# Kernel tuning notes

Measured on AMD Instinct MI355X. Metric: run time of the kernel, lower is better.

The kernel has to match this reference:

```python
import jax, jax.numpy as jnp
import numpy as np

B, N, DIM, PDIM, K = 2, 4096, 512, 64, 16
ALPHA, SIGMA = 0.1, 1.0


def setup_inputs() -> dict:
    key = jax.random.key(0)
    ks = jax.random.split(key, 6)
    sf = 1.0 / np.sqrt(DIM)
    return {
        "states": jax.random.normal(ks[0], (B, N, DIM), jnp.float32),
        "positions": jax.random.normal(ks[1], (B, N, PDIM), jnp.float32),
        "W_flow": jax.random.uniform(ks[2], (PDIM, DIM), jnp.float32, -sf, sf),
        "b_flow": jax.random.uniform(ks[3], (PDIM,), jnp.float32, -sf, sf),
        "W_val": jax.random.uniform(ks[4], (DIM, DIM), jnp.float32, -sf, sf),
        "b_val": jax.random.uniform(ks[5], (DIM,), jnp.float32, -sf, sf),
    }


def _pairwise_dist(p):
    sq = jnp.sum(p * p, axis=-1)  # [B,N]
    d2 = sq[:, :, None] + sq[:, None, :] - 2.0 * jnp.einsum('bnp,bmp->bnm', p, p)
    return jnp.sqrt(jnp.maximum(d2, 1e-12))


def reference(states, positions, W_flow, b_flow, W_val, b_val):
    # flow projection + position update
    flow = jnp.einsum('bnd,pd->bnp', states, W_flow) + b_flow  # [B,N,PDIM]
    new_pos = positions + ALPHA * flow

    # kNN search (exclude self via large diagonal)
    d = _pairwise_dist(new_pos)  # [B,N,N]
    d_knn = d + jnp.eye(N, dtype=d.dtype) * 1e6
    _, nbrs = jax.lax.top_k(-d_knn, K)  # [B,N,K] smallest distances

    # scatter neighbor mask [B,N,N] (no [B,N,K,N] one-hot materialization)
    bidx = jnp.arange(B)[:, None, None]
    ridx = jnp.arange(N)[None, :, None]
    mask = jnp.zeros((B, N, N), d.dtype).at[bidx, ridx, nbrs].set(1.0)

    # gaussian affinities; exp(-d*mask)*mask == exp(-d)*mask on the support
    aff = jnp.exp(-d / (2.0 * SIGMA ** 2)) * mask
    aff = aff / (jnp.sum(aff, axis=-1, keepdims=True) + 1e-8)

    # value projection + weighted aggregation
    values = jnp.einsum('bnd,ed->bne', states, W_val) + b_val  # [B,N,DIM]
    context = jnp.einsum('bnm,bmd->bnd', aff, values)
    return context, new_pos, flow
```

## Files before the change

### kernel.cpp

```cpp
#include <hip/hip_runtime.h>

#define NB 2
#define NN 4096
#define DIMD 512
#define PD 64
#define KNN 16
#define QB 8
#define CAP 192
#define CTRIG 52
#define RCAP 48
#define MROWS (NB*NN)
#define FLOW_BLOCKS (MROWS/4)

typedef unsigned short ushort_t;

__global__ __launch_bounds__(256)
void prep_kernel(const float* __restrict__ states, const float* __restrict__ positions,
                 const float* __restrict__ W_flow, const float* __restrict__ b_flow,
                 const float* __restrict__ W_val, const float* __restrict__ b_val,
                 float* __restrict__ out_np, float* __restrict__ out_fl,
                 float* __restrict__ npos_lo, float* __restrict__ p4t,
                 double* __restrict__ sq64, float* __restrict__ sqf,
                 float* __restrict__ values_ws)
{
    __shared__ __align__(16) unsigned char POOL[24832];
    const int t = threadIdx.x;

    if (blockIdx.x < FLOW_BLOCKS) {
        float (*s_lds)[DIMD] = (float(*)[DIMD])POOL;
        float (*wlds)[65]    = (float(*)[65])(POOL + 8192);
        const int row0 = blockIdx.x * 4;
        const float4* src = (const float4*)(states + (size_t)row0 * DIMD);
        float4* dst = (float4*)&s_lds[0][0];
        dst[t] = src[t];
        dst[t + 256] = src[t + 256];
        const int lr = t >> 6;
        const int p  = t & 63;
        const int row = row0 + lr;
        double a0 = 0.0, a1 = 0.0, a2 = 0.0, a3 = 0.0;
        for (int ph = 0; ph < 8; ++ph) {
            const int d0 = ph << 6;
            __syncthreads();
            #pragma unroll
            for (int i = 0; i < 4; ++i) {
                int slot = t + (i << 8);
                int r = slot >> 4, c = slot & 15;
                float4 wv = *(const float4*)(W_flow + (size_t)r * DIMD + d0 + (c << 2));
                wlds[(c<<2)+0][r] = wv.x;
                wlds[(c<<2)+1][r] = wv.y;
                wlds[(c<<2)+2][r] = wv.z;
                wlds[(c<<2)+3][r] = wv.w;
            }
            __syncthreads();
            #pragma unroll
            for (int sc = 0; sc < 4; ++sc) {
                const int dl = sc << 4;
                float4 s0 = *(const float4*)&s_lds[lr][d0 + dl + 0];
                float4 s1 = *(const float4*)&s_lds[lr][d0 + dl + 4];
                float4 s2 = *(const float4*)&s_lds[lr][d0 + dl + 8];
                float4 s3 = *(const float4*)&s_lds[lr][d0 + dl + 12];
                a0 += (double)s0.x * (double)wlds[dl+ 0][p];
                a1 += (double)s0.y * (double)wlds[dl+ 1][p];
                a2 += (double)s0.z * (double)wlds[dl+ 2][p];
                a3 += (double)s0.w * (double)wlds[dl+ 3][p];
                a0 += (double)s1.x * (double)wlds[dl+ 4][p];
                a1 += (double)s1.y * (double)wlds[dl+ 5][p];
                a2 += (double)s1.z * (double)wlds[dl+ 6][p];
                a3 += (double)s1.w * (double)wlds[dl+ 7][p];
                a0 += (double)s2.x * (double)wlds[dl+ 8][p];
                a1 += (double)s2.y * (double)wlds[dl+ 9][p];
                a2 += (double)s2.z * (double)wlds[dl+10][p];
                a3 += (double)s2.w * (double)wlds[dl+11][p];
                a0 += (double)s3.x * (double)wlds[dl+12][p];
                a1 += (double)s3.y * (double)wlds[dl+13][p];
                a2 += (double)s3.z * (double)wlds[dl+14][p];
                a3 += (double)s3.w * (double)wlds[dl+15][p];
            }
        }
        double acc = ((a0 + a1) + (a2 + a3)) + (double)b_flow[p];
        const size_t g = (size_t)row * PD + p;
        double np_ = (double)positions[g] + 0.1 * acc;
        float hi = (float)np_;
        float lo = (float)(np_ - (double)hi);
        out_fl[g]   = (float)acc;
        out_np[g]   = hi;
        npos_lo[g]  = lo;
        const int bb = row >> 12, n = row & (NN - 1);
        p4t[(((size_t)bb*16 + (p >> 2))*NN + n)*4 + (p & 3)] = hi;
        double s2 = np_ * np_;
        #pragma unroll
        for (int off = 32; off >= 1; off >>= 1) s2 += __shfl_xor(s2, off);
        if (p == 0) { sq64[row] = s2; sqf[row] = (float)s2; }
    } else {
        float (*As)[68] = (float(*)[68])POOL;
        float (*Bs)[68] = (float(*)[68])(POOL + 4352);
        const int idx = blockIdx.x - FLOW_BLOCKS;
        const int bn = idx & 7, bm = idx >> 3;
        const int lr  = t >> 2;
        const int lc4 = (t & 3) << 2;
        const int cr = (t >> 4) << 2;
        const int cc = (t & 15) << 2;
        float acc[4][4] = {};
        for (int k0 = 0; k0 < DIMD; k0 += 16) {
            float4 av = *(const float4*)(states + (size_t)(bm*64 + lr)*DIMD + k0 + lc4);
            float4 wv = *(const float4*)(W_val  + (size_t)(bn*64 + lr)*DIMD + k0 + lc4);
            __syncthreads();
            As[lc4+0][lr] = av.x; As[lc4+1][lr] = av.y; As[lc4+2][lr] = av.z; As[lc4+3][lr] = av.w;
            Bs[lc4+0][lr] = wv.x; Bs[lc4+1][lr] = wv.y; Bs[lc4+2][lr] = wv.z; Bs[lc4+3][lr] = wv.w;
            __syncthreads();
            #pragma unroll
            for (int kk = 0; kk < 16; ++kk) {
                float4 a  = *(const float4*)&As[kk][cr];
                float4 b4 = *(const float4*)&Bs[kk][cc];
                acc[0][0] += a.x*b4.x; acc[0][1] += a.x*b4.y; acc[0][2] += a.x*b4.z; acc[0][3] += a.x*b4.w;
                acc[1][0] += a.y*b4.x; acc[1][1] += a.y*b4.y; acc[1][2] += a.y*b4.z; acc[1][3] += a.y*b4.w;
                acc[2][0] += a.z*b4.x; acc[2][1] += a.z*b4.y; acc[2][2] += a.z*b4.z; acc[2][3] += a.z*b4.w;
                acc[3][0] += a.w*b4.x; acc[3][1] += a.w*b4.y; acc[3][2] += a.w*b4.z; acc[3][3] += a.w*b4.w;
            }
        }
        const int colb = bn*64 + cc;
        float4 bb = *(const float4*)(b_val + colb);
        #pragma unroll
        for (int i = 0; i < 4; ++i) {
            float4 o;
            o.x = acc[i][0] + bb.x;
            o.y = acc[i][1] + bb.y;
            o.z = acc[i][2] + bb.z;
            o.w = acc[i][3] + bb.w;
            *(float4*)(values_ws + (size_t)(bm*64 + cr + i)*DIMD + colb) = o;
        }
    }
}

__global__ __launch_bounds__(256, 4)
void dist_kernel(const float* __restrict__ nph, const float* __restrict__ npl,
                 const float4* __restrict__ p4t, const float* __restrict__ sqf,
                 const double* __restrict__ sq64, const float* __restrict__ values,
                 float* __restrict__ ctx)
{
    __shared__ __align__(16) unsigned char POOL[24576];
    __shared__ float    qstage[QB][68];
    __shared__ ushort_t rlist[QB][4][RCAP];
    __shared__ int      ccnt[QB][4];
    __shared__ int      rcnt[QB][4];

    ushort_t (*sd16)[4][CAP]  = (ushort_t(*)[4][CAP])POOL;
    ushort_t (*six16)[4][CAP] = (ushort_t(*)[4][CAP])(POOL + 12288);
    double (*umbd)[192] = (double(*)[192])POOL;
    int*    umbi        = (int*)(POOL + 12288);
    double (*qd64)[66]  = (double(*)[66])(POOL + 18432);
    int*    fin_ix      = (int*)(POOL + 22656);
    float*  fin_w       = (float*)(POOL + 23168);

    const int tid  = threadIdx.x;
    const int w    = tid >> 6;
    const int lane = tid & 63;
    const int b    = blockIdx.x >> 9;
    const int n0   = (blockIdx.x & 511) << 3;
    const int base = b * NN;

    if (tid < 32) ccnt[tid >> 2][tid & 3] = 0;
    if (tid < 128) {
        int row = tid >> 4, c4 = (tid & 15) << 2;
        *(float4*)&qstage[row][c4] = *(const float4*)(nph + (size_t)(base + n0 + row)*PD + c4);
    }
    __syncthreads();

    float sqq[QB], tv[QB];
    #pragma unroll
    for (int j = 0; j < QB; ++j) { sqq[j] = sqf[base + n0 + j]; tv[j] = 1e30f; }

    const float4* P4 = p4t + (size_t)b * 16 * NN;
    const int qbase = w << 10;

    #define APPEND1(J, DV, CI)                                                  \
        if ((DV) < tv[J]) {                                                     \
            int s_ = atomicAdd(&ccnt[J][w], 1);                                 \
            if (s_ < CAP) {                                                     \
                sd16[J][w][s_]  = (ushort_t)(__float_as_uint(DV) >> 16);        \
                six16[J][w][s_] = (ushort_t)(CI);                               \
            }                                                                   \
        }

    #define COMPACT1(J)                                                         \
        {                                                                       \
            int cnt0 = ccnt[J][w];                                              \
            if (cnt0 > CTRIG) {                                                 \
                if (cnt0 > CAP) cnt0 = CAP;                                     \
                ushort_t v0 = (lane       < cnt0) ? sd16[J][w][lane]       : (ushort_t)0xFFFF; \
                ushort_t v1 = (64 + lane  < cnt0) ? sd16[J][w][64 + lane]  : (ushort_t)0xFFFF; \
                ushort_t v2 = (128 + lane < cnt0) ? sd16[J][w][128 + lane] : (ushort_t)0xFFFF; \
                ushort_t i0 = (lane       < cnt0) ? six16[J][w][lane]       : (ushort_t)0; \
                ushort_t i1 = (64 + lane  < cnt0) ? six16[J][w][64 + lane]  : (ushort_t)0; \
                ushort_t i2 = (128 + lane < cnt0) ? six16[J][w][128 + lane] : (ushort_t)0; \
                unsigned lo_ = 0u, hi_ = 0x7F80u;                               \
                _Pragma("unroll 1")                                             \
                for (int it = 0; it < 16; ++it) {                               \
                    unsigned mid = (lo_ + hi_) >> 1;                            \
                    int cnt = __popcll(__ballot((unsigned)v0 < mid))            \
                            + __popcll(__ballot((unsigned)v1 < mid))            \
                            + __popcll(__ballot((unsigned)v2 < mid));           \
                    if (cnt >= 19) hi_ = mid; else lo_ = mid;                   \
                }                                                               \
                tv[J] = __uint_as_float(hi_ << 16);                             \
                if (lane == 0) ccnt[J][w] = 0;                                  \
                if ((unsigned)v0 < hi_) { int s_ = atomicAdd(&ccnt[J][w], 1); sd16[J][w][s_] = v0; six16[J][w][s_] = i0; } \
                if ((unsigned)v1 < hi_) { int s_ = atomicAdd(&ccnt[J][w], 1); sd16[J][w][s_] = v1; six16[J][w][s_] = i1; } \
                if ((unsigned)v2 < hi_) { int s_ = atomicAdd(&ccnt[J][w], 1); sd16[J][w][s_] = v2; six16[J][w][s_] = i2; } \
            }                                                                   \
        }

    for (int ch = 0; ch < 4; ++ch) {
        const int cbase = qbase + (ch << 8);
        const int c0 = cbase + lane, c1 = c0 + 64, c2 = c0 + 128, c3 = c0 + 192;
        float a[QB][4];
        #pragma unroll
        for (int j = 0; j < QB; ++j) { a[j][0]=0.f; a[j][1]=0.f; a[j][2]=0.f; a[j][3]=0.f; }
        #pragma unroll
        for (int k4 = 0; k4 < 16; ++k4) {
            float4 p0 = P4[(size_t)k4*NN + c0];
            float4 p1 = P4[(size_t)k4*NN + c1];
            float4 p2 = P4[(size_t)k4*NN + c2];
            float4 p3 = P4[(size_t)k4*NN + c3];
            #pragma unroll
            for (int j = 0; j < QB; ++j) {
                float4 qv = *(const float4*)&qstage[j][k4 << 2];
                a[j][0] += qv.x*p0.x + qv.y*p0.y + qv.z*p0.z + qv.w*p0.w;
                a[j][1] += qv.x*p1.x + qv.y*p1.y + qv.z*p1.z + qv.w*p1.w;
                a[j][2] += qv.x*p2.x + qv.y*p2.y + qv.z*p2.z + qv.w*p2.w;
                a[j][3] += qv.x*p3.x + qv.y*p3.y + qv.z*p3.z + qv.w*p3.w;
            }
        }
        const float sc0 = sqf[base + c0], sc1 = sqf[base + c1];
        const float sc2 = sqf[base + c2], sc3 = sqf[base + c3];
        #pragma unroll
        for (int j = 0; j < QB; ++j) {
            float d0 = fmaxf(sqq[j] + sc0 - 2.f*a[j][0], 0.f);
            float d1 = fmaxf(sqq[j] + sc1 - 2.f*a[j][1], 0.f);
            float d2 = fmaxf(sqq[j] + sc2 - 2.f*a[j][2], 0.f);
            float d3 = fmaxf(sqq[j] + sc3 - 2.f*a[j][3], 0.f);
            if (c0 == n0 + j) d0 = 1e30f;
            if (c1 == n0 + j) d1 = 1e30f;
            if (c2 == n0 + j) d2 = 1e30f;
            if (c3 == n0 + j) d3 = 1e30f;
            a[j][0] = d0; a[j][1] = d1; a[j][2] = d2; a[j][3] = d3;
        }

        if (ch == 0) {
            #pragma unroll
            for (int j = 0; j < QB; ++j) {
                unsigned lo = 0u, hi = 0x7F80u;
                #pragma unroll 1
                for (int it = 0; it < 16; ++it) {
                    unsigned mid = (lo + hi) >> 1;
                    float fm = __uint_as_float(mid << 16);
                    int cnt = __popcll(__ballot(a[j][0] < fm)) + __popcll(__ballot(a[j][1] < fm))
                            + __popcll(__ballot(a[j][2] < fm)) + __popcll(__ballot(a[j][3] < fm));
                    if (cnt >= 19) hi = mid; else lo = mid;
                }
                tv[j] = __uint_as_float(hi << 16);
            }
        }

        #pragma unroll
        for (int j = 0; j < QB; ++j) {
            APPEND1(j, a[j][0], c0)
            APPEND1(j, a[j][1], c1)
        }
        #pragma unroll
        for (int j = 0; j < QB; ++j) COMPACT1(j)
        #pragma unroll
        for (int j = 0; j < QB; ++j) {
            APPEND1(j, a[j][2], c2)
            APPEND1(j, a[j][3], c3)
        }
        #pragma unroll
        for (int j = 0; j < QB; ++j) COMPACT1(j)
    }

    if (lane < QB) rcnt[lane][w] = 0;
    #pragma unroll 1
    for (int j = 0; j < QB; ++j) {
        int cnt0 = ccnt[j][w];
        if (cnt0 > CAP) cnt0 = CAP;
        ushort_t v0 = (lane       < cnt0) ? sd16[j][w][lane]       : (ushort_t)0xFFFF;
        ushort_t v1 = (64 + lane  < cnt0) ? sd16[j][w][64 + lane]  : (ushort_t)0xFFFF;
        ushort_t v2 = (128 + lane < cnt0) ? sd16[j][w][128 + lane] : (ushort_t)0xFFFF;
        ushort_t i0 = (lane       < cnt0) ? six16[j][w][lane]       : (ushort_t)0;
        ushort_t i1 = (64 + lane  < cnt0) ? six16[j][w][64 + lane]  : (ushort_t)0;
        ushort_t i2 = (128 + lane < cnt0) ? six16[j][w][128 + lane] : (ushort_t)0;
        unsigned lo = 0u, hi = 0x7F80u;
        #pragma unroll 1
        for (int it = 0; it < 16; ++it) {
            unsigned mid = (lo + hi) >> 1;
            int cnt = __popcll(__ballot((unsigned)v0 < mid))
                    + __popcll(__ballot((unsigned)v1 < mid))
                    + __popcll(__ballot((unsigned)v2 < mid));
            if (cnt >= 20) hi = mid; else lo = mid;
        }
        if ((unsigned)v0 < hi) { int s = atomicAdd(&rcnt[j][w], 1); if (s < RCAP) rlist[j][w][s] = i0; }
        if ((unsigned)v1 < hi) { int s = atomicAdd(&rcnt[j][w], 1); if (s < RCAP) rlist[j][w][s] = i1; }
        if ((unsigned)v2 < hi) { int s = atomicAdd(&rcnt[j][w], 1); if (s < RCAP) rlist[j][w][s] = i2; }
    }
    __syncthreads();

    for (int i = tid; i < QB*PD; i += 256) {
        int q = i >> 6, p = i & 63;
        size_t g = (size_t)(base + n0 + q)*PD + p;
        qd64[q][p] = (double)nph[g] + (double)npl[g];
    }
    for (int i = tid; i < QB*192; i += 256) {
        umbd[i / 192][i % 192] = 1e300;
        umbi[i] = 0x7fffffff;
    }
    __syncthreads();

    const int lh = lane & 15, g4 = lane >> 4;
    #pragma unroll 1
    for (int q = 0; q < QB; ++q) {
        int cr = rcnt[q][w]; if (cr > RCAP) cr = RCAP;
        const double qd0 = qd64[q][4*lh+0], qd1 = qd64[q][4*lh+1];
        const double qd2 = qd64[q][4*lh+2], qd3 = qd64[q][4*lh+3];
        const double sq_q = sq64[base + n0 + q];
        for (int s0 = 0; s0 < cr; s0 += 4) {
            const int slot = s0 + g4;
            const bool valid = slot < cr;
            const int cand = valid ? (int)rlist[q][w][slot] : 0;
            const float4 h4 = *(const float4*)(nph + (size_t)(base + cand)*PD + 4*lh);
            const float4 l4 = *(const float4*)(npl + (size_t)(base + cand)*PD + 4*lh);
            double acc = qd0*((double)h4.x + (double)l4.x)
                       + qd1*((double)h4.y + (double)l4.y)
                       + qd2*((double)h4.z + (double)l4.z)
                       + qd3*((double)h4.w + (double)l4.w);
            #pragma unroll
            for (int off = 1; off < 16; off <<= 1) acc += __shfl_xor(acc, off);
            if (valid && lh == 0) {
                umbd[q][w*RCAP + slot] = sq_q + sq64[base + cand] - 2.0*acc;
                umbi[q*192 + w*RCAP + slot] = cand;
            }
        }
    }
    __syncthreads();

    #pragma unroll 1
    for (int qi = 0; qi < 2; ++qi) {
        const int q = 2*w + qi;
        double ev0 = umbd[q][lane], ev1 = umbd[q][64 + lane], ev2 = umbd[q][128 + lane];
        int ei0 = umbi[q*192 + lane], ei1 = umbi[q*192 + 64 + lane], ei2 = umbi[q*192 + 128 + lane];
        double wsum = 0.0, mywk = 0.0;
        for (int r = 0; r < KNN; ++r) {
            double bv = ev0; int bi = ei0; int bs = 0;
            if (ev1 < bv || (ev1 == bv && ei1 < bi)) { bv = ev1; bi = ei1; bs = 1; }
            if (ev2 < bv || (ev2 == bv && ei2 < bi)) { bv = ev2; bi = ei2; bs = 2; }
            #pragma unroll
            for (int off = 32; off >= 1; off >>= 1) {
                double ov = __shfl_xor(bv, off);
                int    oi = __shfl_xor(bi, off);
                if (ov < bv || (ov == bv && oi < bi)) { bv = ov; bi = oi; }
            }
            if (bs == 0 && ei0 == bi) ev0 = 1e300;
            if (bs == 1 && ei1 == bi) ev1 = 1e300;
            if (bs == 2 && ei2 == bi) ev2 = 1e300;
            double wk = exp(-0.5 * sqrt(fmax(bv, 1e-12)));
            wsum += wk;
            if (lane == r) mywk = wk;
            if (lane == 0) fin_ix[q*16 + r] = bi;
        }
        if (lane < KNN) fin_w[q*16 + lane] = (float)(mywk / (wsum + 1e-8));
    }
    __syncthreads();

    {
        const int q  = tid >> 5;
        const int e0 = (tid & 31) << 4;
        const float* V = values + (size_t)base * DIMD;
        float acc2[16] = {};
        for (int k = 0; k < KNN; ++k) {
            int   m  = fin_ix[q*16 + k];
            float wg = fin_w[q*16 + k];
            const float4* vr = (const float4*)(V + (size_t)m*DIMD + e0);
            #pragma unroll
            for (int t4 = 0; t4 < 4; ++t4) {
                float4 vv = vr[t4];
                acc2[4*t4+0] += wg*vv.x; acc2[4*t4+1] += wg*vv.y;
                acc2[4*t4+2] += wg*vv.z; acc2[4*t4+3] += wg*vv.w;
            }
        }
        float* crow = ctx + (size_t)(base + n0 + q)*DIMD + e0;
        #pragma unroll
        for (int t4 = 0; t4 < 4; ++t4)
            *(float4*)(crow + 4*t4) = make_float4(acc2[4*t4+0], acc2[4*t4+1], acc2[4*t4+2], acc2[4*t4+3]);
    }
    #undef APPEND1
    #undef COMPACT1
}

extern "C" void kernel_launch(void* const* d_in, const int* in_sizes, int n_in,
                              void* d_out, int out_size, void* d_ws, size_t ws_size,
                              hipStream_t stream)
{
    (void)in_sizes; (void)n_in; (void)out_size; (void)ws_size;
    const float* states    = (const float*)d_in[0];
    const float* positions = (const float*)d_in[1];
    const float* W_flow    = (const float*)d_in[2];
    const float* b_flow    = (const float*)d_in[3];
    const float* W_val     = (const float*)d_in[4];
    const float* b_val     = (const float*)d_in[5];

    float* out_ctx = (float*)d_out;
    float* out_np  = out_ctx + (size_t)NB*NN*DIMD;
    float* out_fl  = out_np  + (size_t)NB*NN*PD;

    char* ws = (char*)d_ws;
    float*  values_ws = (float*)ws;
    float*  npos_lo   = (float*)(ws + (size_t)16777216);
    double* sq64      = (double*)(ws + (size_t)18874368);
    float*  sqf       = (float*)(ws + (size_t)18939904);
    float*  p4t       = (float*)(ws + (size_t)18972672);

    hipLaunchKernelGGL(prep_kernel, dim3(FLOW_BLOCKS + (DIMD/64)*(MROWS/64)), dim3(256), 0, stream,
                       states, positions, W_flow, b_flow, W_val, b_val,
                       out_np, out_fl, npos_lo, p4t, sq64, sqf, values_ws);
    hipLaunchKernelGGL(dist_kernel, dim3(NB*512), dim3(256), 0, stream,
                       out_np, npos_lo, (const float4*)p4t, sqf, sq64, values_ws, out_ctx);
}
```

Measured before the change: 316.0 us.

## Split kNN candidate scan across two blocks per query group and merge in a finish kernel

The distance/selection kernel now handles half of the candidate columns per block, doubling the grid to 2048 blocks. Each half writes its 16 best (distance, index) pairs into the context output buffer as scratch. A new finish kernel merges the 32 candidates per query by rank counting, computes normalized Gaussian weights, and aggregates the values rows. This raises parallelism and occupancy for the compute-heavy scan, at the cost of an extra launch and a global round trip through the context buffer.

```diff
diff --git a/kernel.cpp b/kernel.cpp
--- a/kernel.cpp
+++ b/kernel.cpp
@@ -133,10 +133,9 @@
 }
 
 __global__ __launch_bounds__(256, 4)
-void dist_kernel(const float* __restrict__ nph, const float* __restrict__ npl,
+void dist_select(const float* __restrict__ nph, const float* __restrict__ npl,
                  const float4* __restrict__ p4t, const float* __restrict__ sqf,
-                 const double* __restrict__ sq64, const float* __restrict__ values,
-                 float* __restrict__ ctx)
+                 const double* __restrict__ sq64, float* __restrict__ ctx)
 {
     __shared__ __align__(16) unsigned char POOL[24576];
     __shared__ float    qstage[QB][68];
@@ -149,14 +148,14 @@
     double (*umbd)[192] = (double(*)[192])POOL;
     int*    umbi        = (int*)(POOL + 12288);
     double (*qd64)[66]  = (double(*)[66])(POOL + 18432);
-    int*    fin_ix      = (int*)(POOL + 22656);
-    float*  fin_w       = (float*)(POOL + 23168);
 
     const int tid  = threadIdx.x;
     const int w    = tid >> 6;
     const int lane = tid & 63;
-    const int b    = blockIdx.x >> 9;
-    const int n0   = (blockIdx.x & 511) << 3;
+    const int b    = blockIdx.x >> 10;
+    const int rem  = blockIdx.x & 1023;
+    const int n0   = (rem >> 1) << 3;
+    const int half = rem & 1;
     const int base = b * NN;
 
     if (tid < 32) ccnt[tid >> 2][tid & 3] = 0;
@@ -171,7 +170,7 @@
     for (int j = 0; j < QB; ++j) { sqq[j] = sqf[base + n0 + j]; tv[j] = 1e30f; }
 
     const float4* P4 = p4t + (size_t)b * 16 * NN;
-    const int qbase = w << 10;
+    const int qbase = (half << 11) + (w << 9);
 
     #define APPEND1(J, DV, CI)                                                  \
         if ((DV) < tv[J]) {                                                     \
@@ -210,7 +209,7 @@
             }                                                                   \
         }
 
-    for (int ch = 0; ch < 4; ++ch) {
+    for (int ch = 0; ch < 2; ++ch) {
         const int cbase = qbase + (ch << 8);
         const int c0 = cbase + lane, c1 = c0 + 64, c2 = c0 + 128, c3 = c0 + 192;
         float a[QB][4];
@@ -347,7 +346,7 @@
         const int q = 2*w + qi;
         double ev0 = umbd[q][lane], ev1 = umbd[q][64 + lane], ev2 = umbd[q][128 + lane];
         int ei0 = umbi[q*192 + lane], ei1 = umbi[q*192 + 64 + lane], ei2 = umbi[q*192 + 128 + lane];
-        double wsum = 0.0, mywk = 0.0;
+        double myd = 1e300; int myi = 0x7fffffff;
         for (int r = 0; r < KNN; ++r) {
             double bv = ev0; int bi = ei0; int bs = 0;
             if (ev1 < bv || (ev1 == bv && ei1 < bi)) { bv = ev1; bi = ei1; bs = 1; }
@@ -361,12 +360,52 @@
             if (bs == 0 && ei0 == bi) ev0 = 1e300;
             if (bs == 1 && ei1 == bi) ev1 = 1e300;
             if (bs == 2 && ei2 == bi) ev2 = 1e300;
-            double wk = exp(-0.5 * sqrt(fmax(bv, 1e-12)));
-            wsum += wk;
-            if (lane == r) mywk = wk;
-            if (lane == 0) fin_ix[q*16 + r] = bi;
-        }
-        if (lane < KNN) fin_w[q*16 + lane] = (float)(mywk / (wsum + 1e-8));
+            if (lane == r) { myd = bv; myi = bi; }
+        }
+        float* crow = ctx + (size_t)(base + n0 + q)*DIMD;
+        if (lane < KNN) {
+            ((double*)crow)[half*16 + lane]      = myd;
+            ((int*)(crow + 64))[half*16 + lane]  = myi;
+        }
+    }
+    #undef APPEND1
+    #undef COMPACT1
+}
+
+__global__ __launch_bounds__(256)
+void finish_kernel(const float* __restrict__ values, float* __restrict__ ctx)
+{
+    __shared__ int   s_ix[QB][16];
+    __shared__ float s_w[QB][16];
+    const int tid  = threadIdx.x;
+    const int w    = tid >> 6;
+    const int lane = tid & 63;
+    const int b    = blockIdx.x >> 9;
+    const int n0   = (blockIdx.x & 511) << 3;
+    const int base = b * NN;
+
+    {
+        const int sub = lane >> 5, sl = lane & 31;
+        const int q = 2*w + sub;
+        const float* crow = ctx + (size_t)(base + n0 + q)*DIMD;
+        double d2 = ((const double*)crow)[sl];
+        int    ix = ((const int*)(crow + 64))[sl];
+        int rank = 0;
+        #pragma unroll 1
+        for (int j = 0; j < 32; ++j) {
+            double dj = __shfl(d2, j, 32);
+            int    ij = __shfl(ix, j, 32);
+            rank += (dj < d2) || (dj == d2 && ij < ix);
+        }
+        double wk = 0.0;
+        if (rank < KNN) wk = exp(-0.5 * sqrt(fmax(d2, 1e-12)));
+        double ws = wk;
+        #pragma unroll
+        for (int off = 16; off >= 1; off >>= 1) ws += __shfl_xor(ws, off, 32);
+        if (rank < KNN) {
+            s_ix[q][rank] = ix;
+            s_w[q][rank]  = (float)(wk / (ws + 1e-8));
+        }
     }
     __syncthreads();
 
@@ -376,8 +415,8 @@
         const float* V = values + (size_t)base * DIMD;
         float acc2[16] = {};
         for (int k = 0; k < KNN; ++k) {
-            int   m  = fin_ix[q*16 + k];
-            float wg = fin_w[q*16 + k];
+            int   m  = s_ix[q][k];
+            float wg = s_w[q][k];
             const float4* vr = (const float4*)(V + (size_t)m*DIMD + e0);
             #pragma unroll
             for (int t4 = 0; t4 < 4; ++t4) {
@@ -391,8 +430,6 @@
         for (int t4 = 0; t4 < 4; ++t4)
             *(float4*)(crow + 4*t4) = make_float4(acc2[4*t4+0], acc2[4*t4+1], acc2[4*t4+2], acc2[4*t4+3]);
     }
-    #undef APPEND1
-    #undef COMPACT1
 }
 
 extern "C" void kernel_launch(void* const* d_in, const int* in_sizes, int n_in,
@@ -421,6 +458,8 @@
     hipLaunchKernelGGL(prep_kernel, dim3(FLOW_BLOCKS + (DIMD/64)*(MROWS/64)), dim3(256), 0, stream,
                        states, positions, W_flow, b_flow, W_val, b_val,
                        out_np, out_fl, npos_lo, p4t, sq64, sqf, values_ws);
-    hipLaunchKernelGGL(dist_kernel, dim3(NB*512), dim3(256), 0, stream,
-                       out_np, npos_lo, (const float4*)p4t, sqf, sq64, values_ws, out_ctx);
+    hipLaunchKernelGGL(dist_select, dim3(2048), dim3(256), 0, stream,
+                       out_np, npos_lo, (const float4*)p4t, sqf, sq64, out_ctx);
+    hipLaunchKernelGGL(finish_kernel, dim3(1024), dim3(256), 0, stream,
+                       values_ws, out_ctx);
 }
```

After: 392.3 us. +24.2%, slower.
